# Kernel tuning notes

Hardware: AMD Instinct MI355X
Metric: run time of the kernel (lower is better)

The kernel has to match this reference:

```python
import jax, jax.numpy as jnp
import numpy as np

B, T, F, R = 16, 1024, 128, 2048
GAMMA = 0.95
HALF = R // 2


def setup_inputs() -> dict:
    key = jax.random.key(0)
    k1, k2, k3, k4, k5 = jax.random.split(key, 5)
    inputs = jax.random.normal(k1, (B, T, F), dtype=jnp.float32)
    # GlorotNormal for input_weights [R, F]
    std = np.sqrt(2.0 / (R + F)).astype(np.float32)
    input_weights = jax.random.normal(k2, (R, F), dtype=jnp.float32) * std
    # Orthogonal init for recurrent_weights [R, R]
    q, _ = jnp.linalg.qr(jax.random.normal(k3, (R, R), dtype=jnp.float32))
    recurrent_weights = q
    bias = jax.random.uniform(k4, (R,), dtype=jnp.float32, minval=-0.1, maxval=0.1)
    reservoir_start = jax.random.uniform(k5, (R,), dtype=jnp.float32, minval=-0.1, maxval=0.1)
    return {
        'inputs': inputs,
        'input_weights': input_weights,
        'recurrent_weights': recurrent_weights,
        'bias': bias,
        'reservoir_start': reservoir_start,
    }


def reference(inputs, input_weights, recurrent_weights, bias, reservoir_start):
    # inputs: [B, T, F]; state h: [B, R]; output: [B, T, R//2]
    b, t, f = inputs.shape
    r = recurrent_weights.shape[0]
    half = r // 2
    # in_cor zeroes the second half of the projected input
    in_mask = jnp.concatenate([jnp.ones((half,), inputs.dtype), jnp.zeros((half,), inputs.dtype)])
    # precompute input projection for all timesteps: [T, B, R]
    proj = jnp.einsum('btf,rf->tbr', inputs, input_weights) * in_mask
    h0 = jnp.broadcast_to(reservoir_start[None, :], (b, r))

    def step(h, u):
        h_new = (1.0 - GAMMA) * h + GAMMA * jnp.tanh(h @ recurrent_weights.T + u + bias)
        # out_cor = [0 | I] selects second half of the state
        return h_new, h_new[:, half:]

    _, ys = jax.lax.scan(step, h0, proj)  # ys: [T, B, half]
    return jnp.swapaxes(ys, 0, 1)  # [B, T, half]
```

## Files before the change

### kernel.cpp

```cpp
#include <hip/hip_runtime.h>
#include <math.h>

#define BB 16
#define TT 1024
#define FF 128
#define RR 2048
#define HALFR 1024
#define NBLK 256
#define NTHR 512

typedef __attribute__((ext_vector_type(2))) unsigned int u32x2;
typedef __attribute__((ext_vector_type(4))) unsigned int u32x4;
typedef __attribute__((ext_vector_type(8))) short bf16x8;
typedef __attribute__((ext_vector_type(4))) float f32x4;

__device__ __forceinline__ u32x4 ldg_sc4u(const unsigned* base, unsigned voff) {
    u32x4 r;
    asm volatile("global_load_dwordx4 %0, %1, %2 sc0 sc1"
                 : "=v"(r) : "v"(voff), "s"(base) : "memory");
    return r;
}
__device__ __forceinline__ u32x2 ldg_sc2u(const unsigned* base, unsigned voff) {
    u32x2 r;
    asm volatile("global_load_dwordx2 %0, %1, %2 sc0 sc1"
                 : "=v"(r) : "v"(voff), "s"(base) : "memory");
    return r;
}
__device__ __forceinline__ void stg_sc1u(unsigned* base, unsigned voff, unsigned v) {
    asm volatile("global_store_dword %0, %1, %2 sc0 sc1"
                 :: "v"(voff), "v"(v), "s"(base) : "memory");
}
__device__ __forceinline__ void wait_vm0() {
    asm volatile("s_waitcnt vmcnt(0)" ::: "memory");
}

__device__ __forceinline__ bf16x8 as_bf16x8(u32x4 u) {
    union { u32x4 u4; bf16x8 b8; } c; c.u4 = u; return c.b8;
}

__device__ __forceinline__ void split_bf16(float v, unsigned& hh, unsigned& hl) {
    unsigned uh = (__float_as_uint(v) + 0x8000u) & 0xFFFF0000u;
    float rem = v - __uint_as_float(uh);
    unsigned ul = (__float_as_uint(rem) + 0x8000u) & 0xFFFF0000u;
    hh = uh >> 16; hl = ul >> 16;
}
__device__ __forceinline__ unsigned pack_h(float v) {
    unsigned hh, hl; split_bf16(v, hh, hl);
    return (hl << 16) | hh;
}

__global__ void init_state_kernel(unsigned* __restrict__ h, const float* __restrict__ start,
                                  unsigned* __restrict__ bar) {
    int idx = blockIdx.x * blockDim.x + threadIdx.x;
    if (idx < BB * RR) h[idx] = pack_h(start[idx & (RR - 1)]);
    if (idx < 2048) bar[idx] = 0u;
}

__global__ __launch_bounds__(NTHR, 2) void esn_mfma(
    const float* __restrict__ inputs,
    const float* __restrict__ Win,
    const float* __restrict__ Wrec,
    const float* __restrict__ bias,
    unsigned* __restrict__ hA,
    unsigned* __restrict__ hB,
    float* __restrict__ out,
    unsigned* __restrict__ bar,
    const float* __restrict__ start)
{
    __shared__ __align__(16) float sRed[8 * 256];

    const int tid  = threadIdx.x;
    const int lane = tid & 63;
    const int wave = tid >> 6;
    const int bh   = blockIdx.x & 1;
    const int cb   = blockIdx.x >> 1;
    const int rb   = cb * 16;
    const int col  = lane & 15;
    const int kg   = lane >> 4;
    const int ksb  = wave * 256;
    const bool projb = (rb < HALFR);
    const bool mreal = (col < 8);

    bf16x8 Wh[8], Wl[8];
#pragma unroll
    for (int s = 0; s < 8; ++s) {
        const float* wp = Wrec + (size_t)(rb + col) * RR + ksb + s * 32 + kg * 8;
        const float4 w0 = *(const float4*)wp;
        const float4 w1 = *(const float4*)(wp + 4);
        const float wv[8] = {w0.x, w0.y, w0.z, w0.w, w1.x, w1.y, w1.z, w1.w};
        unsigned hh[8], hl[8];
#pragma unroll
        for (int e = 0; e < 8; ++e) split_bf16(wv[e], hh[e], hl[e]);
        u32x4 ph = { hh[0] | (hh[1] << 16), hh[2] | (hh[3] << 16),
                     hh[4] | (hh[5] << 16), hh[6] | (hh[7] << 16) };
        u32x4 pl = { hl[0] | (hl[1] << 16), hl[2] | (hl[3] << 16),
                     hl[4] | (hl[5] << 16), hl[6] | (hl[7] << 16) };
        Wh[s] = as_bf16x8(ph);
        Wl[s] = as_bf16x8(pl);
    }

    bf16x8 Ih = {0,0,0,0,0,0,0,0}, Il = {0,0,0,0,0,0,0,0};
    const bool xwave = projb && (wave < 4);
    if (xwave) {
        const float* ip = Win + (size_t)(rb + col) * FF + wave * 32 + kg * 8;
        const float4 w0 = *(const float4*)ip;
        const float4 w1 = *(const float4*)(ip + 4);
        const float wv[8] = {w0.x, w0.y, w0.z, w0.w, w1.x, w1.y, w1.z, w1.w};
        unsigned hh[8], hl[8];
#pragma unroll
        for (int e = 0; e < 8; ++e) split_bf16(wv[e], hh[e], hl[e]);
        u32x4 ph = { hh[0] | (hh[1] << 16), hh[2] | (hh[3] << 16),
                     hh[4] | (hh[5] << 16), hh[6] | (hh[7] << 16) };
        u32x4 pl = { hl[0] | (hl[1] << 16), hl[2] | (hl[3] << 16),
                     hl[4] | (hl[5] << 16), hl[6] | (hl[7] << 16) };
        Ih = as_bf16x8(ph);
        Il = as_bf16x8(pl);
    }

    const int batm = bh * 8 + (col & 7);
    unsigned voffH[8][2];
#pragma unroll
    for (int s = 0; s < 8; ++s) {
        const unsigned base = (unsigned)(((batm * RR) + ksb + s * 32 + kg * 8) * 4);
        voffH[s][0] = base;
        voffH[s][1] = base + 16;
    }
    const size_t xbase = (size_t)batm * TT * FF + wave * 32 + kg * 8;

    const int mE = tid >> 4;
    const int nE = tid & 15;
    const int eBatch = bh * 8 + (mE & 7);
    const int eCol   = rb + nE;
    const bool ownS  = (tid < 256) && (mE < 8);
    const float myBias = bias[eCol];
    const unsigned eOff = (unsigned)((eBatch * RR + eCol) * 4);
    float holdv = start[eCol];

    const unsigned pollOff = (unsigned)((bh * 128 + lane * 2) * 4);
    const unsigned epOff   = (unsigned)((bh * 128 + cb) * 4);

    float4 xc0 = {0,0,0,0}, xc1 = {0,0,0,0};
    if (xwave && mreal) {
        const float* xp = inputs + xbase;
        xc0 = *(const float4*)xp;
        xc1 = *(const float4*)(xp + 4);
    }

    for (int t = 0; t < TT; ++t) {
        const unsigned tgt = (unsigned)t;
        if (wave == 0) {
            for (;;) {
                u32x2 v = ldg_sc2u(bar, pollOff);
                wait_vm0();
                if (__all((v.x >= tgt) && (v.y >= tgt))) break;
            }
        }
        __syncthreads();

        const unsigned* hc = (t & 1) ? hB : hA;
        unsigned*       hn = (t & 1) ? hA : hB;

        u32x4 hld[16];
        if (mreal) {
#pragma unroll
            for (int s = 0; s < 8; ++s) {
                hld[2 * s]     = ldg_sc4u(hc, voffH[s][0]);
                hld[2 * s + 1] = ldg_sc4u(hc, voffH[s][1]);
            }
        } else {
#pragma unroll
            for (int i = 0; i < 16; ++i) hld[i] = (u32x4){0u, 0u, 0u, 0u};
        }
        float4 xn0 = {0,0,0,0}, xn1 = {0,0,0,0};
        if (xwave && mreal) {
            const int tp1 = (t + 1 < TT) ? (t + 1) : (TT - 1);
            const float* xp = inputs + xbase + (size_t)tp1 * FF;
            xn0 = *(const float4*)xp;
            xn1 = *(const float4*)(xp + 4);
        }

        wait_vm0();
        __builtin_amdgcn_sched_barrier(0);

        f32x4 accA = {0.f, 0.f, 0.f, 0.f};
        f32x4 accB = {0.f, 0.f, 0.f, 0.f};
        f32x4 accC = {0.f, 0.f, 0.f, 0.f};
#pragma unroll
        for (int s = 0; s < 8; ++s) {
            const u32x4 pa = hld[2 * s];
            const u32x4 pb = hld[2 * s + 1];
            u32x4 ahh = { (pa.x & 0xFFFFu) | (pa.y << 16),
                          (pa.z & 0xFFFFu) | (pa.w << 16),
                          (pb.x & 0xFFFFu) | (pb.y << 16),
                          (pb.z & 0xFFFFu) | (pb.w << 16) };
            u32x4 ahl = { (pa.x >> 16) | (pa.y & 0xFFFF0000u),
                          (pa.z >> 16) | (pa.w & 0xFFFF0000u),
                          (pb.x >> 16) | (pb.y & 0xFFFF0000u),
                          (pb.z >> 16) | (pb.w & 0xFFFF0000u) };
            const bf16x8 Ah = as_bf16x8(ahh);
            const bf16x8 Al = as_bf16x8(ahl);
            accA = __builtin_amdgcn_mfma_f32_16x16x32_bf16(Ah, Wh[s], accA, 0, 0, 0);
            accB = __builtin_amdgcn_mfma_f32_16x16x32_bf16(Al, Wh[s], accB, 0, 0, 0);
            accC = __builtin_amdgcn_mfma_f32_16x16x32_bf16(Ah, Wl[s], accC, 0, 0, 0);
        }
        if (xwave) {
            const float xv[8] = {xc0.x, xc0.y, xc0.z, xc0.w, xc1.x, xc1.y, xc1.z, xc1.w};
            unsigned hh[8], hl[8];
#pragma unroll
            for (int e = 0; e < 8; ++e) split_bf16(xv[e], hh[e], hl[e]);
            u32x4 ph = { hh[0] | (hh[1] << 16), hh[2] | (hh[3] << 16),
                         hh[4] | (hh[5] << 16), hh[6] | (hh[7] << 16) };
            u32x4 pl = { hl[0] | (hl[1] << 16), hl[2] | (hl[3] << 16),
                         hl[4] | (hl[5] << 16), hl[6] | (hl[7] << 16) };
            const bf16x8 Axh = as_bf16x8(ph);
            const bf16x8 Axl = as_bf16x8(pl);
            accA = __builtin_amdgcn_mfma_f32_16x16x32_bf16(Axh, Ih, accA, 0, 0, 0);
            accB = __builtin_amdgcn_mfma_f32_16x16x32_bf16(Axl, Ih, accB, 0, 0, 0);
            accC = __builtin_amdgcn_mfma_f32_16x16x32_bf16(Axh, Il, accC, 0, 0, 0);
        }
        const f32x4 acc = accA + accB + accC;

        *(f32x4*)&sRed[wave * 256 + lane * 4] = acc;
        __syncthreads();
        if (tid < 256) {
            const int ridx = ((mE >> 2) * 16 + nE) * 4 + (mE & 3);
            float val = 0.f;
#pragma unroll
            for (int w = 0; w < 8; ++w) val += sRed[w * 256 + ridx];
            if (ownS) {
                const float pre  = val + myBias;
                const float vnew = 0.05f * holdv + 0.95f * tanhf(pre);
                holdv = vnew;
                stg_sc1u(hn, eOff, pack_h(vnew));
                if (eCol >= HALFR)
                    out[((size_t)eBatch * TT + t) * HALFR + (eCol - HALFR)] = vnew;
            }
        }

        wait_vm0();
        __syncthreads();
        if (tid == 0) stg_sc1u(bar, epOff, (unsigned)(t + 1));

        xc0 = xn0; xc1 = xn1;
    }
}


__global__ void init_h_kernel(float* __restrict__ h, const float* __restrict__ start) {
    int idx = blockIdx.x * blockDim.x + threadIdx.x;
    if (idx < BB * RR) h[idx] = start[idx & (RR - 1)];
}

__global__ __launch_bounds__(512, 2) void step_kernel(
    const float* __restrict__ inputs, const float* __restrict__ Win,
    const float* __restrict__ Wrec, const float* __restrict__ bias,
    const float* __restrict__ h_cur, float* __restrict__ h_next,
    float* __restrict__ out, int t)
{
    const int tid  = threadIdx.x;
    const int wave = tid >> 6;
    const int half = (tid >> 5) & 1;
    const int kl   = tid & 31;
    const int b    = wave * 2 + half;
    const int r0   = blockIdx.x * 8;

    float acc[8];
#pragma unroll
    for (int r = 0; r < 8; ++r) acc[r] = 0.0f;

    if (r0 < HALFR) {
        const float4 in4 = *reinterpret_cast<const float4*>(
            inputs + ((size_t)b * TT + t) * FF + kl * 4);
#pragma unroll
        for (int r = 0; r < 8; ++r) {
            const float4 w4 = *reinterpret_cast<const float4*>(
                Win + (size_t)(r0 + r) * FF + kl * 4);
            acc[r] += in4.x * w4.x + in4.y * w4.y + in4.z * w4.z + in4.w * w4.w;
        }
    }

    const float* hb = h_cur + (size_t)b * RR;
#pragma unroll 2
    for (int j = 0; j < 16; ++j) {
        const int k = kl * 4 + j * 128;
        const float4 h4 = *reinterpret_cast<const float4*>(hb + k);
#pragma unroll
        for (int r = 0; r < 8; ++r) {
            const float4 w4 = *reinterpret_cast<const float4*>(
                Wrec + (size_t)(r0 + r) * RR + k);
            acc[r] = fmaf(h4.x, w4.x, acc[r]);
            acc[r] = fmaf(h4.y, w4.y, acc[r]);
            acc[r] = fmaf(h4.z, w4.z, acc[r]);
            acc[r] = fmaf(h4.w, w4.w, acc[r]);
        }
    }

#pragma unroll
    for (int r = 0; r < 8; ++r) {
        float v = acc[r];
        v += __shfl_xor(v, 1);  v += __shfl_xor(v, 2);
        v += __shfl_xor(v, 4);  v += __shfl_xor(v, 8);
        v += __shfl_xor(v, 16);
        acc[r] = v;
    }

    __shared__ float red[BB][8];
    if (kl == 0) {
#pragma unroll
        for (int r = 0; r < 8; ++r) red[b][r] = acc[r];
    }
    __syncthreads();

    if (tid < BB * 8) {
        const int rr = tid & 7, bb = tid >> 3;
        const int r  = r0 + rr;
        const float pre = red[bb][rr] + bias[r];
        const float h_old = h_cur[(size_t)bb * RR + r];
        const float hn = 0.05f * h_old + 0.95f * tanhf(pre);
        h_next[(size_t)bb * RR + r] = hn;
        if (r0 >= HALFR) out[((size_t)bb * TT + t) * HALFR + (r - HALFR)] = hn;
    }
}


extern "C" void kernel_launch(void* const* d_in, const int* in_sizes, int n_in,
                              void* d_out, int out_size, void* d_ws, size_t ws_size,
                              hipStream_t stream) {
    const float* inputs = (const float*)d_in[0];
    const float* Win    = (const float*)d_in[1];
    const float* Wrec   = (const float*)d_in[2];
    const float* bias   = (const float*)d_in[3];
    const float* start  = (const float*)d_in[4];
    float* out = (float*)d_out;

    unsigned* hA = (unsigned*)d_ws;
    unsigned* hB = hA + (size_t)BB * RR;
    unsigned* bar = hB + (size_t)BB * RR;
    const size_t need = (size_t)BB * RR * 4 * 2 + 8192;

    if (ws_size >= need) {
        init_state_kernel<<<64, 512, 0, stream>>>(hA, start, bar);
        void* args[] = { (void*)&inputs, (void*)&Win, (void*)&Wrec, (void*)&bias,
                         (void*)&hA, (void*)&hB, (void*)&out, (void*)&bar,
                         (void*)&start };
        hipLaunchCooperativeKernel((void*)esn_mfma, dim3(NBLK), dim3(NTHR),
                                   args, 0, stream);
    } else {
        float* fA = (float*)d_ws;
        float* fB = fA + (size_t)BB * RR;
        init_h_kernel<<<(BB * RR + 255) / 256, 256, 0, stream>>>(fA, start);
        for (int t = 0; t < TT; ++t) {
            const float* hcur = (t & 1) ? fB : fA;
            float*       hnxt = (t & 1) ? fA : fB;
            step_kernel<<<256, 512, 0, stream>>>(inputs, Win, Wrec, bias, hcur, hnxt, out, t);
        }
    }
}
```

Before: 5.124 ms.

## Repartition ESN blocks to 4 batches x 32 columns with LDS-staged state

Each block now covers 4 batch rows and 32 output columns, instead of 8 batches and 16 columns. Each wave stages the recurrent state through shared memory with coalesced global loads and then reads MFMA A-fragments from LDS. This halves the per-block state traffic and the barrier fan-in, since each poll now checks 64 flags per batch group instead of 128. The next-step input prefetch is dropped, so input loads now sit on the critical path each step. The MFMA rows carry replicated batches, and two of the accumulator chains are merged into one.

```diff
diff --git a/kernel.cpp b/kernel.cpp
--- a/kernel.cpp
+++ b/kernel.cpp
@@ -9,7 +9,6 @@
 #define NBLK 256
 #define NTHR 512
 
-typedef __attribute__((ext_vector_type(2))) unsigned int u32x2;
 typedef __attribute__((ext_vector_type(4))) unsigned int u32x4;
 typedef __attribute__((ext_vector_type(8))) short bf16x8;
 typedef __attribute__((ext_vector_type(4))) float f32x4;
@@ -20,9 +19,9 @@
                  : "=v"(r) : "v"(voff), "s"(base) : "memory");
     return r;
 }
-__device__ __forceinline__ u32x2 ldg_sc2u(const unsigned* base, unsigned voff) {
-    u32x2 r;
-    asm volatile("global_load_dwordx2 %0, %1, %2 sc0 sc1"
+__device__ __forceinline__ unsigned ldg_sc1r(const unsigned* base, unsigned voff) {
+    unsigned r;
+    asm volatile("global_load_dword %0, %1, %2 sc0 sc1"
                  : "=v"(r) : "v"(voff), "s"(base) : "memory");
     return r;
 }
@@ -67,128 +66,120 @@
     unsigned* __restrict__ bar,
     const float* __restrict__ start)
 {
-    __shared__ __align__(16) float sRed[8 * 256];
+    __shared__ __align__(16) unsigned sH[8 * 1024];
+    __shared__ __align__(16) float sRed[16 * 256];
 
     const int tid  = threadIdx.x;
     const int lane = tid & 63;
     const int wave = tid >> 6;
-    const int bh   = blockIdx.x & 1;
-    const int cb   = blockIdx.x >> 1;
-    const int rb   = cb * 16;
+    const int q    = blockIdx.x & 3;
+    const int cb   = blockIdx.x >> 2;
+    const int rb   = cb * 32;
     const int col  = lane & 15;
     const int kg   = lane >> 4;
     const int ksb  = wave * 256;
     const bool projb = (rb < HALFR);
-    const bool mreal = (col < 8);
-
-    bf16x8 Wh[8], Wl[8];
-#pragma unroll
-    for (int s = 0; s < 8; ++s) {
-        const float* wp = Wrec + (size_t)(rb + col) * RR + ksb + s * 32 + kg * 8;
-        const float4 w0 = *(const float4*)wp;
-        const float4 w1 = *(const float4*)(wp + 4);
-        const float wv[8] = {w0.x, w0.y, w0.z, w0.w, w1.x, w1.y, w1.z, w1.w};
-        unsigned hh[8], hl[8];
-#pragma unroll
-        for (int e = 0; e < 8; ++e) split_bf16(wv[e], hh[e], hl[e]);
-        u32x4 ph = { hh[0] | (hh[1] << 16), hh[2] | (hh[3] << 16),
-                     hh[4] | (hh[5] << 16), hh[6] | (hh[7] << 16) };
-        u32x4 pl = { hl[0] | (hl[1] << 16), hl[2] | (hl[3] << 16),
-                     hl[4] | (hl[5] << 16), hl[6] | (hl[7] << 16) };
-        Wh[s] = as_bf16x8(ph);
-        Wl[s] = as_bf16x8(pl);
-    }
-
-    bf16x8 Ih = {0,0,0,0,0,0,0,0}, Il = {0,0,0,0,0,0,0,0};
     const bool xwave = projb && (wave < 4);
+
+    bf16x8 Wh[2][8], Wl[2][8];
+#pragma unroll
+    for (int nt = 0; nt < 2; ++nt)
+#pragma unroll
+        for (int s = 0; s < 8; ++s) {
+            const float* wp = Wrec + (size_t)(rb + nt * 16 + col) * RR + ksb + s * 32 + kg * 8;
+            const float4 w0 = *(const float4*)wp;
+            const float4 w1 = *(const float4*)(wp + 4);
+            const float wv[8] = {w0.x, w0.y, w0.z, w0.w, w1.x, w1.y, w1.z, w1.w};
+            unsigned hh[8], hl[8];
+#pragma unroll
+            for (int e = 0; e < 8; ++e) split_bf16(wv[e], hh[e], hl[e]);
+            u32x4 ph = { hh[0] | (hh[1] << 16), hh[2] | (hh[3] << 16),
+                         hh[4] | (hh[5] << 16), hh[6] | (hh[7] << 16) };
+            u32x4 pl = { hl[0] | (hl[1] << 16), hl[2] | (hl[3] << 16),
+                         hl[4] | (hl[5] << 16), hl[6] | (hl[7] << 16) };
+            Wh[nt][s] = as_bf16x8(ph);
+            Wl[nt][s] = as_bf16x8(pl);
+        }
+
+    bf16x8 Ih[2] = { {0,0,0,0,0,0,0,0}, {0,0,0,0,0,0,0,0} };
+    bf16x8 Il[2] = { {0,0,0,0,0,0,0,0}, {0,0,0,0,0,0,0,0} };
     if (xwave) {
-        const float* ip = Win + (size_t)(rb + col) * FF + wave * 32 + kg * 8;
-        const float4 w0 = *(const float4*)ip;
-        const float4 w1 = *(const float4*)(ip + 4);
-        const float wv[8] = {w0.x, w0.y, w0.z, w0.w, w1.x, w1.y, w1.z, w1.w};
-        unsigned hh[8], hl[8];
-#pragma unroll
-        for (int e = 0; e < 8; ++e) split_bf16(wv[e], hh[e], hl[e]);
-        u32x4 ph = { hh[0] | (hh[1] << 16), hh[2] | (hh[3] << 16),
-                     hh[4] | (hh[5] << 16), hh[6] | (hh[7] << 16) };
-        u32x4 pl = { hl[0] | (hl[1] << 16), hl[2] | (hl[3] << 16),
-                     hl[4] | (hl[5] << 16), hl[6] | (hl[7] << 16) };
-        Ih = as_bf16x8(ph);
-        Il = as_bf16x8(pl);
-    }
-
-    const int batm = bh * 8 + (col & 7);
-    unsigned voffH[8][2];
-#pragma unroll
-    for (int s = 0; s < 8; ++s) {
-        const unsigned base = (unsigned)(((batm * RR) + ksb + s * 32 + kg * 8) * 4);
-        voffH[s][0] = base;
-        voffH[s][1] = base + 16;
-    }
-    const size_t xbase = (size_t)batm * TT * FF + wave * 32 + kg * 8;
-
-    const int mE = tid >> 4;
-    const int nE = tid & 15;
-    const int eBatch = bh * 8 + (mE & 7);
+#pragma unroll
+        for (int nt = 0; nt < 2; ++nt) {
+            const float* ip = Win + (size_t)(rb + nt * 16 + col) * FF + wave * 32 + kg * 8;
+            const float4 w0 = *(const float4*)ip;
+            const float4 w1 = *(const float4*)(ip + 4);
+            const float wv[8] = {w0.x, w0.y, w0.z, w0.w, w1.x, w1.y, w1.z, w1.w};
+            unsigned hh[8], hl[8];
+#pragma unroll
+            for (int e = 0; e < 8; ++e) split_bf16(wv[e], hh[e], hl[e]);
+            u32x4 ph = { hh[0] | (hh[1] << 16), hh[2] | (hh[3] << 16),
+                         hh[4] | (hh[5] << 16), hh[6] | (hh[7] << 16) };
+            u32x4 pl = { hl[0] | (hl[1] << 16), hl[2] | (hl[3] << 16),
+                         hl[4] | (hl[5] << 16), hl[6] | (hl[7] << 16) };
+            Ih[nt] = as_bf16x8(ph);
+            Il[nt] = as_bf16x8(pl);
+        }
+    }
+
+    const unsigned gbase = (unsigned)((((q * 4 + (lane >> 4)) * RR)
+                                       + ksb + (lane & 15) * 16) * 4);
+    const int swb = wave * 1024 + lane * 16;
+    const int srb = wave * 1024 + (col & 3) * 256 + kg * 8;
+
+    const size_t xrow = (size_t)(q * 4 + (col & 3)) * TT * FF + wave * 32 + kg * 8;
+
+    const int mE = tid >> 5;
+    const int nE = tid & 31;
+    const int eBatch = q * 4 + (mE & 3);
     const int eCol   = rb + nE;
-    const bool ownS  = (tid < 256) && (mE < 8);
     const float myBias = bias[eCol];
     const unsigned eOff = (unsigned)((eBatch * RR + eCol) * 4);
     float holdv = start[eCol];
-
-    const unsigned pollOff = (unsigned)((bh * 128 + lane * 2) * 4);
-    const unsigned epOff   = (unsigned)((bh * 128 + cb) * 4);
-
-    float4 xc0 = {0,0,0,0}, xc1 = {0,0,0,0};
-    if (xwave && mreal) {
-        const float* xp = inputs + xbase;
-        xc0 = *(const float4*)xp;
-        xc1 = *(const float4*)(xp + 4);
-    }
+    const int ntE  = nE >> 4;
+    const int ridx = (nE & 15) * 4 + (mE & 3);
+
+    const unsigned pollOff = (unsigned)((q * 64 + lane) * 4);
+    const unsigned epOff   = (unsigned)((q * 64 + cb) * 4);
 
     for (int t = 0; t < TT; ++t) {
         const unsigned tgt = (unsigned)t;
+        const unsigned* hc = (t & 1) ? hB : hA;
+        unsigned*       hn = (t & 1) ? hA : hB;
+
         if (wave == 0) {
             for (;;) {
-                u32x2 v = ldg_sc2u(bar, pollOff);
+                const unsigned v = ldg_sc1r(bar, pollOff);
                 wait_vm0();
-                if (__all((v.x >= tgt) && (v.y >= tgt))) break;
+                if (__all((int)(v >= tgt))) break;
             }
         }
         __syncthreads();
 
-        const unsigned* hc = (t & 1) ? hB : hA;
-        unsigned*       hn = (t & 1) ? hA : hB;
-
-        u32x4 hld[16];
-        if (mreal) {
-#pragma unroll
-            for (int s = 0; s < 8; ++s) {
-                hld[2 * s]     = ldg_sc4u(hc, voffH[s][0]);
-                hld[2 * s + 1] = ldg_sc4u(hc, voffH[s][1]);
-            }
-        } else {
-#pragma unroll
-            for (int i = 0; i < 16; ++i) hld[i] = (u32x4){0u, 0u, 0u, 0u};
-        }
-        float4 xn0 = {0,0,0,0}, xn1 = {0,0,0,0};
-        if (xwave && mreal) {
-            const int tp1 = (t + 1 < TT) ? (t + 1) : (TT - 1);
-            const float* xp = inputs + xbase + (size_t)tp1 * FF;
-            xn0 = *(const float4*)xp;
-            xn1 = *(const float4*)(xp + 4);
-        }
-
+        u32x4 g0 = ldg_sc4u(hc, gbase);
+        u32x4 g1 = ldg_sc4u(hc, gbase + 16u);
+        u32x4 g2 = ldg_sc4u(hc, gbase + 32u);
+        u32x4 g3 = ldg_sc4u(hc, gbase + 48u);
+        float4 xc0 = {0,0,0,0}, xc1 = {0,0,0,0};
+        if (xwave) {
+            const float* xp = inputs + xrow + (size_t)t * FF;
+            xc0 = *(const float4*)xp;
+            xc1 = *(const float4*)(xp + 4);
+        }
         wait_vm0();
         __builtin_amdgcn_sched_barrier(0);
 
-        f32x4 accA = {0.f, 0.f, 0.f, 0.f};
-        f32x4 accB = {0.f, 0.f, 0.f, 0.f};
-        f32x4 accC = {0.f, 0.f, 0.f, 0.f};
+        *(u32x4*)&sH[swb]      = g0;
+        *(u32x4*)&sH[swb + 4]  = g1;
+        *(u32x4*)&sH[swb + 8]  = g2;
+        *(u32x4*)&sH[swb + 12] = g3;
+
+        f32x4 accA[2] = { {0.f,0.f,0.f,0.f}, {0.f,0.f,0.f,0.f} };
+        f32x4 accX[2] = { {0.f,0.f,0.f,0.f}, {0.f,0.f,0.f,0.f} };
 #pragma unroll
         for (int s = 0; s < 8; ++s) {
-            const u32x4 pa = hld[2 * s];
-            const u32x4 pb = hld[2 * s + 1];
+            const u32x4 pa = *(const u32x4*)&sH[srb + s * 32];
+            const u32x4 pb = *(const u32x4*)&sH[srb + s * 32 + 4];
             u32x4 ahh = { (pa.x & 0xFFFFu) | (pa.y << 16),
                           (pa.z & 0xFFFFu) | (pa.w << 16),
                           (pb.x & 0xFFFFu) | (pb.y << 16),
@@ -199,9 +190,12 @@
                           (pb.z >> 16) | (pb.w & 0xFFFF0000u) };
             const bf16x8 Ah = as_bf16x8(ahh);
             const bf16x8 Al = as_bf16x8(ahl);
-            accA = __builtin_amdgcn_mfma_f32_16x16x32_bf16(Ah, Wh[s], accA, 0, 0, 0);
-            accB = __builtin_amdgcn_mfma_f32_16x16x32_bf16(Al, Wh[s], accB, 0, 0, 0);
-            accC = __builtin_amdgcn_mfma_f32_16x16x32_bf16(Ah, Wl[s], accC, 0, 0, 0);
+#pragma unroll
+            for (int nt = 0; nt < 2; ++nt) {
+                accA[nt] = __builtin_amdgcn_mfma_f32_16x16x32_bf16(Ah, Wh[nt][s], accA[nt], 0, 0, 0);
+                accX[nt] = __builtin_amdgcn_mfma_f32_16x16x32_bf16(Al, Wh[nt][s], accX[nt], 0, 0, 0);
+                accX[nt] = __builtin_amdgcn_mfma_f32_16x16x32_bf16(Ah, Wl[nt][s], accX[nt], 0, 0, 0);
+            }
         }
         if (xwave) {
             const float xv[8] = {xc0.x, xc0.y, xc0.z, xc0.w, xc1.x, xc1.y, xc1.z, xc1.w};
@@ -214,34 +208,33 @@
                          hl[4] | (hl[5] << 16), hl[6] | (hl[7] << 16) };
             const bf16x8 Axh = as_bf16x8(ph);
             const bf16x8 Axl = as_bf16x8(pl);
-            accA = __builtin_amdgcn_mfma_f32_16x16x32_bf16(Axh, Ih, accA, 0, 0, 0);
-            accB = __builtin_amdgcn_mfma_f32_16x16x32_bf16(Axl, Ih, accB, 0, 0, 0);
-            accC = __builtin_amdgcn_mfma_f32_16x16x32_bf16(Axh, Il, accC, 0, 0, 0);
-        }
-        const f32x4 acc = accA + accB + accC;
-
-        *(f32x4*)&sRed[wave * 256 + lane * 4] = acc;
+#pragma unroll
+            for (int nt = 0; nt < 2; ++nt) {
+                accA[nt] = __builtin_amdgcn_mfma_f32_16x16x32_bf16(Axh, Ih[nt], accA[nt], 0, 0, 0);
+                accX[nt] = __builtin_amdgcn_mfma_f32_16x16x32_bf16(Axl, Ih[nt], accX[nt], 0, 0, 0);
+                accX[nt] = __builtin_amdgcn_mfma_f32_16x16x32_bf16(Axh, Il[nt], accX[nt], 0, 0, 0);
+            }
+        }
+
+        *(f32x4*)&sRed[(wave * 2 + 0) * 256 + lane * 4] = accA[0] + accX[0];
+        *(f32x4*)&sRed[(wave * 2 + 1) * 256 + lane * 4] = accA[1] + accX[1];
         __syncthreads();
-        if (tid < 256) {
-            const int ridx = ((mE >> 2) * 16 + nE) * 4 + (mE & 3);
+
+        if (tid < 128) {
             float val = 0.f;
 #pragma unroll
-            for (int w = 0; w < 8; ++w) val += sRed[w * 256 + ridx];
-            if (ownS) {
-                const float pre  = val + myBias;
-                const float vnew = 0.05f * holdv + 0.95f * tanhf(pre);
-                holdv = vnew;
-                stg_sc1u(hn, eOff, pack_h(vnew));
-                if (eCol >= HALFR)
-                    out[((size_t)eBatch * TT + t) * HALFR + (eCol - HALFR)] = vnew;
-            }
+            for (int w = 0; w < 8; ++w) val += sRed[(w * 2 + ntE) * 256 + ridx];
+            const float pre  = val + myBias;
+            const float vnew = 0.05f * holdv + 0.95f * tanhf(pre);
+            holdv = vnew;
+            stg_sc1u(hn, eOff, pack_h(vnew));
+            if (eCol >= HALFR)
+                out[((size_t)eBatch * TT + t) * HALFR + (eCol - HALFR)] = vnew;
         }
 
         wait_vm0();
         __syncthreads();
         if (tid == 0) stg_sc1u(bar, epOff, (unsigned)(t + 1));
-
-        xc0 = xn0; xc1 = xn1;
     }
 }
 
```

Result: faster. 4.955 ms (-3.3%).
